# Optimization experiments

Measured on AMD Instinct MI355X. Metric: run time of the kernel, lower is better.

Reference implementation:

```python
import math
import jax, jax.numpy as jnp
import numpy as np

C = 8.0  # decay constant from __init__
_MIN_RAD, _MAX_RAD = 0.9, 0.999


def block_diag_linear(x, w):
    # x: (B,T,D), w: (H, bs, bs) with D = H*bs
    B, T, D = x.shape
    H, bs, _ = w.shape
    xh = x.reshape(B, T, H, bs)
    return jnp.einsum('bthd,hde->bthe', xh, w).reshape(B, T, D)


def linear_scan(a, b):
    # h_t = a_t * h_{t-1} + b_t, h_{-1}=0, via associative scan:
    # (a1,b1) o (a2,b2) = (a1*a2, a2*b1 + b2)
    def op(l, r):
        a1, b1 = l
        a2, b2 = r
        return (a1 * a2, a2 * b1 + b2)
    return jax.lax.associative_scan(op, (a, b), axis=1)[1]


def setup_inputs() -> dict:
    key = jax.random.key(0)
    k1, k2, k3, k4 = jax.random.split(key, 4)
    B, T, D, H = 4, 4096, 1024, 8
    bs = D // H
    x = jax.random.normal(k1, (B, T, D), dtype=jnp.float32)
    std = 1.0 / math.sqrt(bs)
    w_in = jax.random.normal(k2, (H, bs, bs), dtype=jnp.float32) * std
    w_a = jax.random.normal(k3, (H, bs, bs), dtype=jnp.float32) * std
    # a_param init: softplus^{-1} of uniform in [-log(max_rad)/c, -log(min_rad)/c]
    sp = jax.random.uniform(k4, (D,), dtype=jnp.float32,
                            minval=-math.log(_MAX_RAD) / C,
                            maxval=-math.log(_MIN_RAD) / C)
    a_param = jnp.log(jnp.exp(sp) - 1.0 + 1e-8)
    return {"x": x, "a_param": a_param, "w_in": w_in, "w_a": w_a}


def reference(x, a_param, w_in, w_a):
    # RG-LRU forward with h_prev = None
    gate_x = jax.nn.sigmoid(block_diag_linear(x, w_in))  # input gate i_t
    gate_a = jax.nn.sigmoid(block_diag_linear(x, w_a))   # recurrence gate r_t
    log_a = -C * jax.nn.softplus(a_param) * gate_a       # (B,T,D)
    a = jnp.exp(log_a)
    multiplier = jnp.sqrt(1.0 - jnp.exp(2.0 * log_a))    # sqrt(1 - a^2)
    b = multiplier * (gate_x * x)
    y = linear_scan(a, b)                                 # (B,T,D)
    h_last = y[:, -1, :]
    return y, h_last
```

## Files before the change

### kernel.cpp

```cpp
#include <hip/hip_runtime.h>

#define B_ 4
#define T_ 4096
#define D_ 1024
#define H_ 8
#define CL2_ 16
#define NC2_ (T_/CL2_)
#define M_ (B_*T_)

typedef unsigned short u16;
typedef unsigned int u32;
typedef __attribute__((ext_vector_type(8))) short s16x8;
typedef __attribute__((ext_vector_type(4))) float f32x4;

#define LOG2E 1.4426950408889634f

__device__ __forceinline__ float ex2(float x){
#if __has_builtin(__builtin_amdgcn_exp2f)
  return __builtin_amdgcn_exp2f(x);
#else
  return exp2f(x);
#endif
}
__device__ __forceinline__ float rcpf(float x){
#if __has_builtin(__builtin_amdgcn_rcpf)
  return __builtin_amdgcn_rcpf(x);
#else
  return __fdividef(1.0f, x);
#endif
}
__device__ __forceinline__ float bf2f(u16 u){
  union { u32 i; float f; } v; v.i = ((u32)u) << 16; return v.f;
}
__device__ __forceinline__ u16 f2bf(float f){
  union { float f; u32 i; } v; v.f = f;
  u32 i = v.i;
  return (u16)((i + 0x7FFFu + ((i >> 16) & 1u)) >> 16);
}
__device__ __forceinline__ float sigf(float z){
  return rcpf(1.0f + ex2(-LOG2E * z));
}
__device__ __forceinline__ s16x8 cvt8(float4 a, float4 b){
  s16x8 r;
  r[0] = (short)(__float_as_uint(a.x) >> 16);
  r[1] = (short)(__float_as_uint(a.y) >> 16);
  r[2] = (short)(__float_as_uint(a.z) >> 16);
  r[3] = (short)(__float_as_uint(a.w) >> 16);
  r[4] = (short)(__float_as_uint(b.x) >> 16);
  r[5] = (short)(__float_as_uint(b.y) >> 16);
  r[6] = (short)(__float_as_uint(b.z) >> 16);
  r[7] = (short)(__float_as_uint(b.w) >> 16);
  return r;
}

__global__ __launch_bounds__(256) void k0_transpose(const float* __restrict__ w_in,
                                                    const float* __restrict__ w_a,
                                                    u16* __restrict__ wt){
  __shared__ float ls[128][132];
  const int blk = blockIdx.x;
  const float* src = (blk < 8 ? w_in : w_a) + (size_t)(blk & 7) * 128 * 128;
  u16* dst = wt + (size_t)blk * 128 * 128;
  const int tid = threadIdx.x;
  const int r0 = tid >> 5;
  const int c0 = (tid & 31) * 4;
  #pragma unroll
  for (int it = 0; it < 16; ++it){
    int r = r0 + it * 8;
    *(float4*)(&ls[r][c0]) = *(const float4*)(src + r * 128 + c0);
  }
  __syncthreads();
  #pragma unroll
  for (int it = 0; it < 16; ++it){
    int e = r0 + it * 8;
    ushort4 u;
    u.x = f2bf(ls[c0 + 0][e]);
    u.y = f2bf(ls[c0 + 1][e]);
    u.z = f2bf(ls[c0 + 2][e]);
    u.w = f2bf(ls[c0 + 3][e]);
    *(ushort4*)(dst + e * 128 + c0) = u;
  }
}

__global__ __launch_bounds__(256, 2) void k1_gemm(const float* __restrict__ x,
                                                  const float* __restrict__ a_param,
                                                  const u16* __restrict__ wt,
                                                  u32* __restrict__ pack,
                                                  float* __restrict__ carA,
                                                  float* __restrict__ carY){
  __shared__ u16 wtS[2][64][136];
  __shared__ float aspS[64];

  const int blk = blockIdx.x;
  const int h = blk & 7;
  const int eh = (blk >> 3) & 1;
  const int mbase = (blk >> 4) * 128;
  const int tid = threadIdx.x;
  const int wv = tid >> 6, lane = tid & 63;
  const int q = lane >> 4, l = lane & 15;

  {
    uint4 wbuf[8];
    #pragma unroll
    for (int it = 0; it < 8; ++it){
      int idx = tid + it * 256;
      int row = idx >> 4;
      int mat = row >> 6, e = row & 63;
      int c8 = (idx & 15) * 8;
      wbuf[it] = *(const uint4*)(wt + (size_t)mat * (8 * 128 * 128)
                                  + (h * 128 + eh * 64 + e) * 128 + c8);
    }
    #pragma unroll
    for (int it = 0; it < 8; ++it){
      int idx = tid + it * 256;
      int row = idx >> 4;
      int c8 = (idx & 15) * 8;
      *(uint4*)(&wtS[0][0][0] + row * 136 + c8) = wbuf[it];
    }
  }

  const float* xr0 = x + (size_t)(mbase + wv * 32 + l) * D_ + h * 128;
  const float* xr1 = xr0 + 16 * D_;
  float4 A0[4][2], A1[4][2];
  #pragma unroll
  for (int kb = 0; kb < 4; ++kb){
    int ko = kb * 32 + q * 8;
    A0[kb][0] = *(const float4*)(xr0 + ko);
    A0[kb][1] = *(const float4*)(xr0 + ko + 4);
    A1[kb][0] = *(const float4*)(xr1 + ko);
    A1[kb][1] = *(const float4*)(xr1 + ko + 4);
  }

  if (tid < 64){
    float ap = a_param[h * 128 + eh * 64 + tid];
    aspS[tid] = 8.0f * log1pf(__expf(ap));
  }
  __syncthreads();

  f32x4 accX[2][4], accA[2][4];
  #pragma unroll
  for (int mt = 0; mt < 2; ++mt)
    #pragma unroll
    for (int nt = 0; nt < 4; ++nt){ accX[mt][nt] = (f32x4)0.0f; accA[mt][nt] = (f32x4)0.0f; }

  #pragma unroll
  for (int kb = 0; kb < 4; ++kb){
    const int ko = kb * 32 + q * 8;
    s16x8 a0 = cvt8(A0[kb][0], A0[kb][1]);
    s16x8 a1 = cvt8(A1[kb][0], A1[kb][1]);
    #pragma unroll
    for (int nt = 0; nt < 4; ++nt){
      s16x8 bi = *(const s16x8*)(&wtS[0][nt * 16 + l][ko]);
      s16x8 ba = *(const s16x8*)(&wtS[1][nt * 16 + l][ko]);
      accX[0][nt] = __builtin_amdgcn_mfma_f32_16x16x32_bf16(a0, bi, accX[0][nt], 0, 0, 0);
      accX[1][nt] = __builtin_amdgcn_mfma_f32_16x16x32_bf16(a1, bi, accX[1][nt], 0, 0, 0);
      accA[0][nt] = __builtin_amdgcn_mfma_f32_16x16x32_bf16(a0, ba, accA[0][nt], 0, 0, 0);
      accA[1][nt] = __builtin_amdgcn_mfma_f32_16x16x32_bf16(a1, ba, accA[1][nt], 0, 0, 0);
    }
  }

  const int batch = mbase >> 12;
  const int cwb = ((mbase & (T_ - 1)) >> 4) + wv * 2;
  #pragma unroll
  for (int mt = 0; mt < 2; ++mt){
    const int R0 = wv * 32 + mt * 16;
    #pragma unroll
    for (int nt = 0; nt < 4; ++nt){
      const int el = nt * 16 + l;
      const int col = eh * 64 + el;
      const float asp = aspS[el];
      float av[4], bvv[4];
      #pragma unroll
      for (int r = 0; r < 4; ++r){
        const int row = R0 + q * 4 + r;
        float gx = sigf(accX[mt][nt][r]);
        float ga = sigf(accA[mt][nt][r]);
        float la = -asp * ga;
        float a  = ex2(LOG2E * la);
        float mult = sqrtf(fmaxf(1.0f - a * a, 0.0f));
        float xv = x[(size_t)(mbase + row) * D_ + h * 128 + col];
        float bv = mult * gx * xv;
        av[r] = a; bvv[r] = bv;
        pack[(mbase + row) * D_ + h * 128 + col] =
            (u32)f2bf(la) | ((u32)f2bf(bv) << 16);
      }
      float A = av[0] * av[1] * av[2] * av[3];
      float Y = bvv[0];
      Y = fmaf(av[1], Y, bvv[1]);
      Y = fmaf(av[2], Y, bvv[2]);
      Y = fmaf(av[3], Y, bvv[3]);
      float Ap = __shfl_xor(A, 16, 64);
      float Yp = __shfl_xor(Y, 16, 64);
      Y = (lane & 16) ? fmaf(A, Yp, Y) : fmaf(Ap, Y, Yp);
      A *= Ap;
      Ap = __shfl_xor(A, 32, 64);
      Yp = __shfl_xor(Y, 32, 64);
      Y = (lane & 32) ? fmaf(A, Yp, Y) : fmaf(Ap, Y, Yp);
      A *= Ap;
      if ((lane & 48) == 0){
        int ci = (batch * NC2_ + cwb + mt) * D_ + h * 128 + eh * 64 + nt * 16 + l;
        carA[ci] = A;
        carY[ci] = Y;
      }
    }
  }
}

__global__ __launch_bounds__(256) void k3_scan_carries(const float* __restrict__ carA,
                                                       const float* __restrict__ carY,
                                                       float* __restrict__ hin,
                                                       float* __restrict__ hlast){
  const int g = blockIdx.x * 256 + threadIdx.x;
  const int batch = g >> 10, d = g & 1023;
  float hcur = 0.0f;
  #pragma unroll 16
  for (int c = 0; c < NC2_; ++c){
    int ci = (batch * NC2_ + c) * D_ + d;
    float A = carA[ci], Y = carY[ci];
    hin[ci] = hcur;
    hcur = fmaf(A, hcur, Y);
  }
  hlast[batch * D_ + d] = hcur;
}

__global__ __launch_bounds__(256) void k2b_scan(const u32* pack,
                                               const float* __restrict__ hin,
                                               float* y_out){
  const int cg = blockIdx.x;
  const int d0 = threadIdx.x * 4;
  const int base = cg * (CL2_ * D_) + d0;
  float4 yv = *(const float4*)(&hin[cg * D_ + d0]);
  #pragma unroll
  for (int t = 0; t < CL2_; ++t){
    int idx = base + t * D_;
    uint4 w = *(const uint4*)(&pack[idx]);
    float a0 = ex2(LOG2E * bf2f((u16)(w.x & 0xFFFFu)));
    float a1 = ex2(LOG2E * bf2f((u16)(w.y & 0xFFFFu)));
    float a2 = ex2(LOG2E * bf2f((u16)(w.z & 0xFFFFu)));
    float a3 = ex2(LOG2E * bf2f((u16)(w.w & 0xFFFFu)));
    yv.x = fmaf(a0, yv.x, bf2f((u16)(w.x >> 16)));
    yv.y = fmaf(a1, yv.y, bf2f((u16)(w.y >> 16)));
    yv.z = fmaf(a2, yv.z, bf2f((u16)(w.z >> 16)));
    yv.w = fmaf(a3, yv.w, bf2f((u16)(w.w >> 16)));
    *(float4*)(&y_out[idx]) = yv;
  }
}

extern "C" void kernel_launch(void* const* d_in, const int* in_sizes, int n_in,
                              void* d_out, int out_size, void* d_ws, size_t ws_size,
                              hipStream_t stream) {
  const float* x    = (const float*)d_in[0];
  const float* ap   = (const float*)d_in[1];
  const float* w_in = (const float*)d_in[2];
  const float* w_a  = (const float*)d_in[3];
  float* y = (float*)d_out;
  float* hlast = y + (size_t)B_ * T_ * D_;
  u32* pack = (u32*)d_out;

  char* ws = (char*)d_ws;
  u16*   wt   = (u16*)(ws);
  float* carA = (float*)(ws + 524288);
  float* carY = (float*)(ws + 524288 + 4194304);
  float* hin  = (float*)(ws + 524288 + 8388608);

  k0_transpose<<<16, 256, 0, stream>>>(w_in, w_a, wt);
  k1_gemm<<<(M_ / 128) * H_ * 2, 256, 0, stream>>>(x, ap, wt, pack, carA, carY);
  k3_scan_carries<<<16, 256, 0, stream>>>(carA, carY, hin, hlast);
  k2b_scan<<<B_ * NC2_, 256, 0, stream>>>(pack, hin, y);
}
```

Measured before the change: 185.6 us.

## Fuse GEMM, carry scan and output scan into one decoupled-lookback kernel

Merges the gate GEMM, the carry scan and the chunk-local scan into a single kernel. Blocks take their tile index from an atomic ticket and pass per-chunk aggregates and inclusive prefixes to later blocks through flags, using decoupled lookback. This removes the packed intermediate round trip through global memory and two kernel launches. In exchange, blocks may spin-wait on predecessors, and a memset is added to clear the flags each call.

```diff
diff --git a/kernel.cpp b/kernel.cpp
--- a/kernel.cpp
+++ b/kernel.cpp
@@ -4,8 +4,6 @@
 #define T_ 4096
 #define D_ 1024
 #define H_ 8
-#define CL2_ 16
-#define NC2_ (T_/CL2_)
 #define M_ (B_*T_)
 
 typedef unsigned short u16;
@@ -14,6 +12,7 @@
 typedef __attribute__((ext_vector_type(4))) float f32x4;
 
 #define LOG2E 1.4426950408889634f
+#define SC_AGENT __HIP_MEMORY_SCOPE_AGENT
 
 __device__ __forceinline__ float ex2(float x){
 #if __has_builtin(__builtin_amdgcn_exp2f)
@@ -81,20 +80,33 @@
   }
 }
 
-__global__ __launch_bounds__(256, 2) void k1_gemm(const float* __restrict__ x,
-                                                  const float* __restrict__ a_param,
-                                                  const u16* __restrict__ wt,
-                                                  u32* __restrict__ pack,
-                                                  float* __restrict__ carA,
-                                                  float* __restrict__ carY){
-  __shared__ u16 wtS[2][64][136];
+__global__ __launch_bounds__(256, 2) void k1_fused(
+    const float* __restrict__ x, const float* __restrict__ a_param,
+    const u16* __restrict__ wt, int* __restrict__ ticket,
+    u32* __restrict__ flags, float* __restrict__ aggA,
+    float* __restrict__ aggY, float* __restrict__ incV,
+    float* __restrict__ y_out, float* __restrict__ hlast)
+{
+  __shared__ __align__(16) union SMem {
+    u16 w[2][64][136];
+    float y[128 * 68];
+  } SU;
+  __shared__ float waveC[4][64][2];
+  __shared__ float hinS[64];
   __shared__ float aspS[64];
-
-  const int blk = blockIdx.x;
-  const int h = blk & 7;
-  const int eh = (blk >> 3) & 1;
-  const int mbase = (blk >> 4) * 128;
+  __shared__ int vidS;
+
   const int tid = threadIdx.x;
+  if (tid == 0) vidS = atomicAdd(ticket, 1);
+  __syncthreads();
+  const int vid  = vidS;
+  const int mbg  = vid >> 4;
+  const int hh   = vid & 15;
+  const int h = hh >> 1, eh = hh & 1;
+  const int batch = mbg >> 5;
+  const int link  = mbg & 31;
+  const int ch    = batch * 16 + hh;
+  const int mbase = mbg * 128;
   const int wv = tid >> 6, lane = tid & 63;
   const int q = lane >> 4, l = lane & 15;
 
@@ -114,7 +126,7 @@
       int idx = tid + it * 256;
       int row = idx >> 4;
       int c8 = (idx & 15) * 8;
-      *(uint4*)(&wtS[0][0][0] + row * 136 + c8) = wbuf[it];
+      *(uint4*)(&SU.w[0][0][0] + row * 136 + c8) = wbuf[it];
     }
   }
 
@@ -129,18 +141,15 @@
     A1[kb][0] = *(const float4*)(xr1 + ko);
     A1[kb][1] = *(const float4*)(xr1 + ko + 4);
   }
-
-  if (tid < 64){
-    float ap = a_param[h * 128 + eh * 64 + tid];
-    aspS[tid] = 8.0f * log1pf(__expf(ap));
-  }
-  __syncthreads();
-
-  f32x4 accX[2][4], accA[2][4];
+  if (tid < 64)
+    aspS[tid] = 8.0f * log1pf(__expf(a_param[h * 128 + eh * 64 + tid]));
+  __syncthreads();
+
+  f32x4 accX[2][4], accG[2][4];
   #pragma unroll
   for (int mt = 0; mt < 2; ++mt)
     #pragma unroll
-    for (int nt = 0; nt < 4; ++nt){ accX[mt][nt] = (f32x4)0.0f; accA[mt][nt] = (f32x4)0.0f; }
+    for (int nt = 0; nt < 4; ++nt){ accX[mt][nt] = (f32x4)0.0f; accG[mt][nt] = (f32x4)0.0f; }
 
   #pragma unroll
   for (int kb = 0; kb < 4; ++kb){
@@ -149,99 +158,164 @@
     s16x8 a1 = cvt8(A1[kb][0], A1[kb][1]);
     #pragma unroll
     for (int nt = 0; nt < 4; ++nt){
-      s16x8 bi = *(const s16x8*)(&wtS[0][nt * 16 + l][ko]);
-      s16x8 ba = *(const s16x8*)(&wtS[1][nt * 16 + l][ko]);
+      s16x8 bi = *(const s16x8*)(&SU.w[0][nt * 16 + l][ko]);
+      s16x8 ba = *(const s16x8*)(&SU.w[1][nt * 16 + l][ko]);
       accX[0][nt] = __builtin_amdgcn_mfma_f32_16x16x32_bf16(a0, bi, accX[0][nt], 0, 0, 0);
       accX[1][nt] = __builtin_amdgcn_mfma_f32_16x16x32_bf16(a1, bi, accX[1][nt], 0, 0, 0);
-      accA[0][nt] = __builtin_amdgcn_mfma_f32_16x16x32_bf16(a0, ba, accA[0][nt], 0, 0, 0);
-      accA[1][nt] = __builtin_amdgcn_mfma_f32_16x16x32_bf16(a1, ba, accA[1][nt], 0, 0, 0);
-    }
-  }
-
-  const int batch = mbase >> 12;
-  const int cwb = ((mbase & (T_ - 1)) >> 4) + wv * 2;
+      accG[0][nt] = __builtin_amdgcn_mfma_f32_16x16x32_bf16(a0, ba, accG[0][nt], 0, 0, 0);
+      accG[1][nt] = __builtin_amdgcn_mfma_f32_16x16x32_bf16(a1, ba, accG[1][nt], 0, 0, 0);
+    }
+  }
+
+  float av[2][4][4], bv[2][4][4];
   #pragma unroll
   for (int mt = 0; mt < 2; ++mt){
-    const int R0 = wv * 32 + mt * 16;
     #pragma unroll
     for (int nt = 0; nt < 4; ++nt){
       const int el = nt * 16 + l;
       const int col = eh * 64 + el;
       const float asp = aspS[el];
-      float av[4], bvv[4];
       #pragma unroll
       for (int r = 0; r < 4; ++r){
-        const int row = R0 + q * 4 + r;
+        const int row = wv * 32 + mt * 16 + q * 4 + r;
         float gx = sigf(accX[mt][nt][r]);
-        float ga = sigf(accA[mt][nt][r]);
+        float ga = sigf(accG[mt][nt][r]);
         float la = -asp * ga;
         float a  = ex2(LOG2E * la);
         float mult = sqrtf(fmaxf(1.0f - a * a, 0.0f));
         float xv = x[(size_t)(mbase + row) * D_ + h * 128 + col];
-        float bv = mult * gx * xv;
-        av[r] = a; bvv[r] = bv;
-        pack[(mbase + row) * D_ + h * 128 + col] =
-            (u32)f2bf(la) | ((u32)f2bf(bv) << 16);
-      }
-      float A = av[0] * av[1] * av[2] * av[3];
-      float Y = bvv[0];
-      Y = fmaf(av[1], Y, bvv[1]);
-      Y = fmaf(av[2], Y, bvv[2]);
-      Y = fmaf(av[3], Y, bvv[3]);
-      float Ap = __shfl_xor(A, 16, 64);
-      float Yp = __shfl_xor(Y, 16, 64);
-      Y = (lane & 16) ? fmaf(A, Yp, Y) : fmaf(Ap, Y, Yp);
-      A *= Ap;
-      Ap = __shfl_xor(A, 32, 64);
-      Yp = __shfl_xor(Y, 32, 64);
-      Y = (lane & 32) ? fmaf(A, Yp, Y) : fmaf(Ap, Y, Yp);
-      A *= Ap;
-      if ((lane & 48) == 0){
-        int ci = (batch * NC2_ + cwb + mt) * D_ + h * 128 + eh * 64 + nt * 16 + l;
-        carA[ci] = A;
-        carY[ci] = Y;
-      }
-    }
-  }
-}
-
-__global__ __launch_bounds__(256) void k3_scan_carries(const float* __restrict__ carA,
-                                                       const float* __restrict__ carY,
-                                                       float* __restrict__ hin,
-                                                       float* __restrict__ hlast){
-  const int g = blockIdx.x * 256 + threadIdx.x;
-  const int batch = g >> 10, d = g & 1023;
-  float hcur = 0.0f;
-  #pragma unroll 16
-  for (int c = 0; c < NC2_; ++c){
-    int ci = (batch * NC2_ + c) * D_ + d;
-    float A = carA[ci], Y = carY[ci];
-    hin[ci] = hcur;
-    hcur = fmaf(A, hcur, Y);
-  }
-  hlast[batch * D_ + d] = hcur;
-}
-
-__global__ __launch_bounds__(256) void k2b_scan(const u32* pack,
-                                               const float* __restrict__ hin,
-                                               float* y_out){
-  const int cg = blockIdx.x;
-  const int d0 = threadIdx.x * 4;
-  const int base = cg * (CL2_ * D_) + d0;
-  float4 yv = *(const float4*)(&hin[cg * D_ + d0]);
-  #pragma unroll
-  for (int t = 0; t < CL2_; ++t){
-    int idx = base + t * D_;
-    uint4 w = *(const uint4*)(&pack[idx]);
-    float a0 = ex2(LOG2E * bf2f((u16)(w.x & 0xFFFFu)));
-    float a1 = ex2(LOG2E * bf2f((u16)(w.y & 0xFFFFu)));
-    float a2 = ex2(LOG2E * bf2f((u16)(w.z & 0xFFFFu)));
-    float a3 = ex2(LOG2E * bf2f((u16)(w.w & 0xFFFFu)));
-    yv.x = fmaf(a0, yv.x, bf2f((u16)(w.x >> 16)));
-    yv.y = fmaf(a1, yv.y, bf2f((u16)(w.y >> 16)));
-    yv.z = fmaf(a2, yv.z, bf2f((u16)(w.z >> 16)));
-    yv.w = fmaf(a3, yv.w, bf2f((u16)(w.w >> 16)));
-    *(float4*)(&y_out[idx]) = yv;
+        av[mt][nt][r] = a;
+        bv[mt][nt][r] = mult * gx * xv;
+      }
+    }
+  }
+
+  float preA[2][4], preY[2][4];
+  #pragma unroll
+  for (int nt = 0; nt < 4; ++nt){
+    const int col = nt * 16 + l;
+    float S0A = 1.0f, S0Y = 0.0f;
+    #pragma unroll
+    for (int mt = 0; mt < 2; ++mt){
+      float a0 = av[mt][nt][0], a1 = av[mt][nt][1], a2 = av[mt][nt][2], a3 = av[mt][nt][3];
+      float b0 = bv[mt][nt][0], b1 = bv[mt][nt][1], b2 = bv[mt][nt][2], b3 = bv[mt][nt][3];
+      float TA = (a0 * a1) * (a2 * a3);
+      float TY = fmaf(a3, fmaf(a2, fmaf(a1, b0, b1), b2), b3);
+      float QA0 = __shfl(TA, l,      64), QY0 = __shfl(TY, l,      64);
+      float QA1 = __shfl(TA, l + 16, 64), QY1 = __shfl(TY, l + 16, 64);
+      float QA2 = __shfl(TA, l + 32, 64), QY2 = __shfl(TY, l + 32, 64);
+      float QA3 = __shfl(TA, l + 48, 64), QY3 = __shfl(TY, l + 48, 64);
+      float P1A = QA0,       P1Y = QY0;
+      float P2A = P1A * QA1, P2Y = fmaf(QA1, P1Y, QY1);
+      float P3A = P2A * QA2, P3Y = fmaf(QA2, P2Y, QY2);
+      float QpA = (q == 0) ? 1.0f : ((q == 1) ? P1A : ((q == 2) ? P2A : P3A));
+      float QpY = (q == 0) ? 0.0f : ((q == 1) ? P1Y : ((q == 2) ? P2Y : P3Y));
+      float S16A = P3A * QA3, S16Y = fmaf(QA3, P3Y, QY3);
+      float MA = (mt == 0) ? 1.0f : S0A;
+      float MY = (mt == 0) ? 0.0f : S0Y;
+      preA[mt][nt] = MA * QpA;
+      preY[mt][nt] = fmaf(QpA, MY, QpY);
+      if (mt == 0){ S0A = S16A; S0Y = S16Y; }
+      else {
+        float WA = S0A * S16A, WY = fmaf(S16A, S0Y, S16Y);
+        if (lane < 16){ waveC[wv][col][0] = WA; waveC[wv][col][1] = WY; }
+      }
+    }
+  }
+  __syncthreads();
+
+  float wpA[4], wpY[4];
+  #pragma unroll
+  for (int nt = 0; nt < 4; ++nt){
+    int col = nt * 16 + l;
+    float A = 1.0f, Y = 0.0f;
+    #pragma unroll
+    for (int w2 = 0; w2 < 3; ++w2){
+      if (w2 < wv){
+        float cA = waveC[w2][col][0], cY = waveC[w2][col][1];
+        Y = fmaf(cA, Y, cY);
+        A = A * cA;
+      }
+    }
+    wpA[nt] = A; wpY[nt] = Y;
+  }
+
+  if (wv == 0){
+    const int col = lane;
+    float c0A = waveC[0][col][0], c0Y = waveC[0][col][1];
+    float c1A = waveC[1][col][0], c1Y = waveC[1][col][1];
+    float c2A = waveC[2][col][0], c2Y = waveC[2][col][1];
+    float c3A = waveC[3][col][0], c3Y = waveC[3][col][1];
+    float bA = c0A * c1A,  bY = fmaf(c1A, c0Y, c1Y);
+    bY = fmaf(c2A, bY, c2Y); bA *= c2A;
+    bY = fmaf(c3A, bY, c3Y); bA *= c3A;
+    float hprev = 0.0f;
+    const int base = (ch * 32 + link) * 64 + col;
+    if (link > 0){
+      __hip_atomic_store(&aggA[base], bA, __ATOMIC_RELAXED, SC_AGENT);
+      __hip_atomic_store(&aggY[base], bY, __ATOMIC_RELAXED, SC_AGENT);
+      if (lane == 0)
+        __hip_atomic_store(&flags[ch * 32 + link], 1u, __ATOMIC_RELEASE, SC_AGENT);
+      float acA = 1.0f, acY = 0.0f;
+      int j = link - 1;
+      while (true){
+        u32 f;
+        do {
+          f = __hip_atomic_load(&flags[ch * 32 + j], __ATOMIC_ACQUIRE, SC_AGENT);
+          if (f == 0) __builtin_amdgcn_s_sleep(2);
+        } while (f == 0);
+        const int cj = (ch * 32 + j) * 64 + col;
+        if (f == 2u){
+          float hj = __hip_atomic_load(&incV[cj], __ATOMIC_RELAXED, SC_AGENT);
+          hprev = fmaf(acA, hj, acY);
+          break;
+        } else {
+          float aA = __hip_atomic_load(&aggA[cj], __ATOMIC_RELAXED, SC_AGENT);
+          float aY = __hip_atomic_load(&aggY[cj], __ATOMIC_RELAXED, SC_AGENT);
+          acY = fmaf(acA, aY, acY);
+          acA = acA * aA;
+          --j;
+        }
+      }
+    }
+    float hout = fmaf(bA, hprev, bY);
+    __hip_atomic_store(&incV[base], hout, __ATOMIC_RELAXED, SC_AGENT);
+    if (lane == 0)
+      __hip_atomic_store(&flags[ch * 32 + link], 2u, __ATOMIC_RELEASE, SC_AGENT);
+    hinS[col] = hprev;
+    if (link == 31) hlast[batch * D_ + h * 128 + eh * 64 + col] = hout;
+  }
+  __syncthreads();
+
+  float* yS = SU.y;
+  #pragma unroll
+  for (int nt = 0; nt < 4; ++nt){
+    const int col = nt * 16 + l;
+    float h0 = hinS[col];
+    float basev = fmaf(wpA[nt], h0, wpY[nt]);
+    #pragma unroll
+    for (int mt = 0; mt < 2; ++mt){
+      float v = fmaf(preA[mt][nt], basev, preY[mt][nt]);
+      const int R0 = wv * 32 + mt * 16 + q * 4;
+      #pragma unroll
+      for (int r = 0; r < 4; ++r){
+        v = fmaf(av[mt][nt][r], v, bv[mt][nt][r]);
+        yS[(R0 + r) * 68 + col] = v;
+      }
+    }
+  }
+  __syncthreads();
+
+  {
+    float* yg = y_out + (size_t)mbase * D_ + h * 128 + eh * 64;
+    #pragma unroll
+    for (int it = 0; it < 8; ++it){
+      int idx = tid + it * 256;
+      int row = idx >> 4;
+      int c4 = (idx & 15) * 4;
+      float4 v = *(float4*)(&yS[row * 68 + c4]);
+      *(float4*)(yg + (size_t)row * D_ + c4) = v;
+    }
   }
 }
 
@@ -254,16 +328,17 @@
   const float* w_a  = (const float*)d_in[3];
   float* y = (float*)d_out;
   float* hlast = y + (size_t)B_ * T_ * D_;
-  u32* pack = (u32*)d_out;
 
   char* ws = (char*)d_ws;
-  u16*   wt   = (u16*)(ws);
-  float* carA = (float*)(ws + 524288);
-  float* carY = (float*)(ws + 524288 + 4194304);
-  float* hin  = (float*)(ws + 524288 + 8388608);
-
+  u16*   wt     = (u16*)(ws);
+  u32*   flags  = (u32*)(ws + 524288);
+  int*   ticket = (int*)(ws + 524288 + 8192);
+  float* aggA   = (float*)(ws + 540672);
+  float* aggY   = (float*)(ws + 540672 + 524288);
+  float* incV   = (float*)(ws + 540672 + 1048576);
+
+  hipMemsetAsync(ws + 524288, 0, 8448, stream);
   k0_transpose<<<16, 256, 0, stream>>>(w_in, w_a, wt);
-  k1_gemm<<<(M_ / 128) * H_ * 2, 256, 0, stream>>>(x, ap, wt, pack, carA, carY);
-  k3_scan_carries<<<16, 256, 0, stream>>>(carA, carY, hin, hlast);
-  k2b_scan<<<B_ * NC2_, 256, 0, stream>>>(pack, hin, y);
-}
+  k1_fused<<<2048, 256, 0, stream>>>(x, ap, wt, ticket, flags, aggA, aggY, incV,
+                                     y, hlast);
+}
```

After: 339.0 us. 1.83x slower.
